# Kernel optimization log

Hardware: AMD Instinct MI355X
Metric: run time of the kernel (lower is better)

The kernel has to match this reference:

```python
import jax, jax.numpy as jnp
import numpy as np

B, N, C = 8, 2048, 512  # batch, points, channels; dk == C


def _mlp(x, W, b):
    # torch MLP helper = Linear followed by ReLU (even on the last layer)
    return jax.nn.relu(x @ W + b)


def setup_inputs() -> dict:
    key = jax.random.key(0)
    ks = jax.random.split(key, 5)
    s = 1.0 / np.sqrt(C)
    return {
        "x": jax.random.normal(ks[0], (B, N, C), dtype=jnp.float32),
        "Wh": jax.random.normal(ks[1], (C, C), dtype=jnp.float32) * s,
        "bh": jnp.zeros((C,), dtype=jnp.float32),
        "Wl": jax.random.normal(ks[2], (C, C), dtype=jnp.float32) * s,
        "bl": jnp.zeros((C,), dtype=jnp.float32),
        "Wg": jax.random.normal(ks[3], (C, C), dtype=jnp.float32) * s,
        "bg": jnp.zeros((C,), dtype=jnp.float32),
        "Wm": jax.random.normal(ks[4], (C, C), dtype=jnp.float32) * s,
        "bm": jnp.zeros((C,), dtype=jnp.float32),
    }


def reference(x, Wh, bh, Wl, bl, Wg, bg, Wm, bm):
    h = _mlp(x, Wh, bh)                      # [B, N, dk] (torch transposes; folded into einsum)
    l = _mlp(x, Wl, bl)                      # [B, N, dk]
    scores = jnp.einsum("bnd,bmd->bnm", l, h)  # [B, N, N]
    attn = jax.nn.softmax(scores, axis=-1)
    g = _mlp(x, Wg, bg)                      # [B, N, C]
    out = x + jnp.einsum("bnm,bmc->bnc", attn, g)
    return _mlp(out, Wm, bm)
```

## Files before the change

kernel.cpp:

```cpp
#include <hip/hip_runtime.h>


typedef __attribute__((ext_vector_type(4))) float f32x4;
typedef __attribute__((ext_vector_type(8))) short s16x8;
typedef __attribute__((ext_vector_type(8))) _Float16 f16x8;

typedef unsigned int u32;
typedef __attribute__((address_space(1))) const u32 gu32;
typedef __attribute__((address_space(3))) u32 lu32;

__device__ __forceinline__ void gload16(const short* g, short* l) {
  __builtin_amdgcn_global_load_lds((gu32*)g, (lu32*)l, 16, 0, 0);
}

__device__ __forceinline__ short f2h(float f) {
  _Float16 h = (_Float16)f;
  return __builtin_bit_cast(short, h);
}

#define MFMA(a, b, c) __builtin_amdgcn_mfma_f32_16x16x32_f16(a, b, c, 0, 0, 0)


__global__ __launch_bounds__(256) void conv_x_kernel(const float* __restrict__ x,
                                                     short* __restrict__ xb) {
  int i = blockIdx.x * 256 + threadIdx.x;
  const float4* xv = (const float4*)x;
  float4 a = xv[2 * i], b = xv[2 * i + 1];
  s16x8 o;
  o[0] = f2h(a.x); o[1] = f2h(a.y); o[2] = f2h(a.z); o[3] = f2h(a.w);
  o[4] = f2h(b.x); o[5] = f2h(b.y); o[6] = f2h(b.z); o[7] = f2h(b.w);
  ((s16x8*)xb)[i] = o;
}

__global__ __launch_bounds__(256) void conv_w_kernel(const float* __restrict__ Wh,
                                                     const float* __restrict__ Wl,
                                                     const float* __restrict__ Wg,
                                                     const float* __restrict__ Wm,
                                                     short* __restrict__ Wt) {
  int idx = blockIdx.x * 256 + threadIdx.x;
  int k = idx & 511, n = (idx >> 9) & 511, w = idx >> 18;
  const float* W = (w == 0) ? Wh : (w == 1) ? Wl : (w == 2) ? Wg : Wm;
  Wt[idx] = f2h(W[k * 512 + n]);
}


__global__ __launch_bounds__(256) void mlp3_kernel(const short* __restrict__ A,
                                                   const short* __restrict__ Wt_all,
                                                   const float* __restrict__ bh,
                                                   const float* __restrict__ bl,
                                                   const float* __restrict__ bg,
                                                   short* __restrict__ h,
                                                   short* __restrict__ l,
                                                   short* __restrict__ gT) {
  int z = blockIdx.z;
  const short* Wt = Wt_all + z * 262144;
  const float* bias = (z == 0) ? bh : (z == 1) ? bl : bg;

  __shared__ __align__(16) short lds_a[128 * 40];
  __shared__ __align__(16) short lds_b[128 * 40];
  int tid = threadIdx.x, lane = tid & 63, w = tid >> 6;
  int wm = w >> 1, wn = w & 1;
  int bm = blockIdx.x * 128, bn = blockIdx.y * 128;

  f32x4 acc[4][4];
#pragma unroll
  for (int mi = 0; mi < 4; ++mi)
#pragma unroll
    for (int ni = 0; ni < 4; ++ni) acc[mi][ni] = (f32x4){0.f, 0.f, 0.f, 0.f};

  for (int k0 = 0; k0 < 512; k0 += 32) {
#pragma unroll
    for (int it = 0; it < 2; ++it) {
      int chunk = tid + it * 256;
      int row = chunk >> 2, c8 = (chunk & 3) * 8;
      *(s16x8*)&lds_a[row * 40 + c8] =
          *(const s16x8*)&A[(size_t)(bm + row) * 512 + k0 + c8];
      *(s16x8*)&lds_b[row * 40 + c8] =
          *(const s16x8*)&Wt[(bn + row) * 512 + k0 + c8];
    }
    __syncthreads();
    f16x8 af[4], bfr[4];
#pragma unroll
    for (int mi = 0; mi < 4; ++mi)
      af[mi] = *(const f16x8*)&lds_a[(wm * 64 + mi * 16 + (lane & 15)) * 40 +
                                     (lane >> 4) * 8];
#pragma unroll
    for (int ni = 0; ni < 4; ++ni)
      bfr[ni] = *(const f16x8*)&lds_b[(wn * 64 + ni * 16 + (lane & 15)) * 40 +
                                      (lane >> 4) * 8];
#pragma unroll
    for (int mi = 0; mi < 4; ++mi)
#pragma unroll
      for (int ni = 0; ni < 4; ++ni) acc[mi][ni] = MFMA(af[mi], bfr[ni], acc[mi][ni]);
    __syncthreads();
  }

#pragma unroll
  for (int mi = 0; mi < 4; ++mi)
#pragma unroll
    for (int ni = 0; ni < 4; ++ni) {
      int col = bn + wn * 64 + ni * 16 + (lane & 15);
      float bv = bias[col];
#pragma unroll
      for (int r = 0; r < 4; ++r) {
        int row = bm + wm * 64 + mi * 16 + (lane >> 4) * 4 + r;
        float v = fmaxf(acc[mi][ni][r] + bv, 0.0f);
        short o = f2h(v);
        if (z == 0) h[(size_t)row * 512 + col] = o;
        else if (z == 1) l[(size_t)row * 512 + col] = o;
        else {
          int bb = row >> 11, mm = row & 2047;
          gT[((size_t)bb * 512 + col) * 2048 + mm] = o;
        }
      }
    }
}


__global__ __launch_bounds__(256, 1) void attn_kernel(const short* __restrict__ lmat,
                                                      const short* __restrict__ hmat,
                                                      const short* __restrict__ gT,
                                                      const float* __restrict__ x,
                                                      short* __restrict__ y) {
  __shared__ __align__(16) short kbuf[2][16384];
  __shared__ __align__(16) short gbuf[2][16384];
  __shared__ __align__(16) short lds_p[4][512];
  int tid = threadIdx.x, lane = tid & 63, w = tid >> 6;
  int swz = (blockIdx.x & 7) * 32 + (blockIdx.x >> 3);
  int b = swz >> 5, qt = swz & 31;
  int q0 = qt * 64 + w * 16;
  const short* lb = lmat + (size_t)b * 2048 * 512;
  const short* hb = hmat + (size_t)b * 2048 * 512;
  const short* gb = gT + (size_t)b * 512 * 2048;

  int r0 = lane & 15, g = lane >> 4;

  f16x8 qf[16];
  {
    int q = q0 + r0;
#pragma unroll
    for (int ks = 0; ks < 16; ++ks)
      qf[ks] = *(const f16x8*)&lb[(size_t)q * 512 + ks * 32 + g * 8];
  }
  f32x4 accO[32];
#pragma unroll
  for (int i = 0; i < 32; ++i) accO[i] = (f32x4){0.f, 0.f, 0.f, 0.f};
  float mrun[4], lsumL[4];
#pragma unroll
  for (int r = 0; r < 4; ++r) { mrun[r] = -3e38f; lsumL[r] = 0.f; }

  auto stage = [&](int buf, int t) {
    int key0 = t * 32;
    short* kd = &kbuf[buf][0];
    short* gd = &gbuf[buf][0];
#pragma unroll
    for (int j = 0; j < 8; ++j) {
      int wl = w * 8 + j;
      gload16(hb + (size_t)(key0 + wl) * 512 + (((lane * 16) ^ ((wl & 7) << 4)) >> 1),
              kd + wl * 512);
      int c = wl * 16 + (lane >> 2);
      gload16(gb + (size_t)c * 2048 + key0 + (lane & 3) * 8,
              gd + wl * 512);
    }
  };

  stage(0, 0);
  __syncthreads();
  int cur = 0;

  for (int kt = 0; kt < 64; ++kt) {
    if (kt < 63) stage(cur ^ 1, kt + 1);

    const short* kb = &kbuf[cur][0];
    const short* gp = &gbuf[cur][0];

    f32x4 s0 = {0.f, 0.f, 0.f, 0.f}, s1 = {0.f, 0.f, 0.f, 0.f};
#pragma unroll
    for (int ks = 0; ks < 16; ++ks) {
      f16x8 k0f = *(const f16x8*)&kb[(r0 * 512 + ks * 32 + g * 8) ^ ((r0 & 7) << 3)];
      s0 = MFMA(qf[ks], k0f, s0);
      f16x8 k1f = *(const f16x8*)&kb[((r0 + 16) * 512 + ks * 32 + g * 8) ^ ((r0 & 7) << 3)];
      s1 = MFMA(qf[ks], k1f, s1);
    }

    float mnew[4];
    bool ok = true;
#pragma unroll
    for (int r = 0; r < 4; ++r) {
      float m2 = fmaxf(s0[r], s1[r]);
#pragma unroll
      for (int m = 1; m < 16; m <<= 1) m2 = fmaxf(m2, __shfl_xor(m2, m));
      mnew[r] = fmaxf(mrun[r], m2);
      ok = ok && (m2 <= mrun[r] + 8.0f);
    }
    if (!__all((int)ok)) {
      float sc[4];
#pragma unroll
      for (int r = 0; r < 4; ++r) {
        sc[r] = __expf(mrun[r] - mnew[r]);
        mrun[r] = mnew[r];
        lsumL[r] *= sc[r];
      }
#pragma unroll
      for (int nf = 0; nf < 32; ++nf) {
        accO[nf][0] *= sc[0]; accO[nf][1] *= sc[1];
        accO[nf][2] *= sc[2]; accO[nf][3] *= sc[3];
      }
    }
#pragma unroll
    for (int r = 0; r < 4; ++r) {
      float p0 = __expf(s0[r] - mrun[r]);
      float p1 = __expf(s1[r] - mrun[r]);
      int qr = g * 4 + r;
      lds_p[w][qr * 32 + r0] = f2h(p0);
      lds_p[w][qr * 32 + 16 + r0] = f2h(p1);
      lsumL[r] += p0 + p1;
    }

    f16x8 pa = *(const f16x8*)&lds_p[w][r0 * 32 + g * 8];
#pragma unroll
    for (int nf = 0; nf < 32; ++nf) {
      f16x8 gf = *(const f16x8*)&gp[(nf * 16 + r0) * 32 + g * 8];
      accO[nf] = MFMA(pa, gf, accO[nf]);
    }

    __syncthreads();
    cur ^= 1;
  }

  float lsum[4];
#pragma unroll
  for (int r = 0; r < 4; ++r) {
    float s = lsumL[r];
#pragma unroll
    for (int m = 1; m < 16; m <<= 1) s += __shfl_xor(s, m);
    lsum[r] = s;
  }
#pragma unroll
  for (int nf = 0; nf < 32; ++nf) {
    int c = nf * 16 + r0;
#pragma unroll
    for (int r = 0; r < 4; ++r) {
      int q = q0 + g * 4 + r;
      float v = accO[nf][r] / lsum[r];
      v += x[((size_t)b * 2048 + q) * 512 + c];
      y[((size_t)b * 2048 + q) * 512 + c] = f2h(v);
    }
  }
}


__global__ __launch_bounds__(256) void final_gemm_kernel(const short* __restrict__ A,
                                                         const short* __restrict__ Wt,
                                                         const float* __restrict__ bias,
                                                         float* __restrict__ out) {
  __shared__ __align__(16) short lds_a[128 * 40];
  __shared__ __align__(16) short lds_b[128 * 40];
  int tid = threadIdx.x, lane = tid & 63, w = tid >> 6;
  int wm = w >> 1, wn = w & 1;
  int bm = blockIdx.x * 128, bn = blockIdx.y * 128;

  f32x4 acc[4][4];
#pragma unroll
  for (int mi = 0; mi < 4; ++mi)
#pragma unroll
    for (int ni = 0; ni < 4; ++ni) acc[mi][ni] = (f32x4){0.f, 0.f, 0.f, 0.f};

  for (int k0 = 0; k0 < 512; k0 += 32) {
#pragma unroll
    for (int it = 0; it < 2; ++it) {
      int chunk = tid + it * 256;
      int row = chunk >> 2, c8 = (chunk & 3) * 8;
      *(s16x8*)&lds_a[row * 40 + c8] =
          *(const s16x8*)&A[(size_t)(bm + row) * 512 + k0 + c8];
      *(s16x8*)&lds_b[row * 40 + c8] =
          *(const s16x8*)&Wt[(bn + row) * 512 + k0 + c8];
    }
    __syncthreads();
    f16x8 af[4], bfr[4];
#pragma unroll
    for (int mi = 0; mi < 4; ++mi)
      af[mi] = *(const f16x8*)&lds_a[(wm * 64 + mi * 16 + (lane & 15)) * 40 +
                                     (lane >> 4) * 8];
#pragma unroll
    for (int ni = 0; ni < 4; ++ni)
      bfr[ni] = *(const f16x8*)&lds_b[(wn * 64 + ni * 16 + (lane & 15)) * 40 +
                                      (lane >> 4) * 8];
#pragma unroll
    for (int mi = 0; mi < 4; ++mi)
#pragma unroll
      for (int ni = 0; ni < 4; ++ni) acc[mi][ni] = MFMA(af[mi], bfr[ni], acc[mi][ni]);
    __syncthreads();
  }

#pragma unroll
  for (int mi = 0; mi < 4; ++mi)
#pragma unroll
    for (int ni = 0; ni < 4; ++ni) {
      int col = bn + wn * 64 + ni * 16 + (lane & 15);
      float bv = bias[col];
#pragma unroll
      for (int r = 0; r < 4; ++r) {
        int row = bm + wm * 64 + mi * 16 + (lane >> 4) * 4 + r;
        out[(size_t)row * 512 + col] = fmaxf(acc[mi][ni][r] + bv, 0.0f);
      }
    }
}


extern "C" void kernel_launch(void* const* d_in, const int* in_sizes, int n_in,
                              void* d_out, int out_size, void* d_ws, size_t ws_size,
                              hipStream_t stream) {
  const float* x  = (const float*)d_in[0];
  const float* Wh = (const float*)d_in[1];
  const float* bh = (const float*)d_in[2];
  const float* Wl = (const float*)d_in[3];
  const float* bl = (const float*)d_in[4];
  const float* Wg = (const float*)d_in[5];
  const float* bg = (const float*)d_in[6];
  const float* Wm = (const float*)d_in[7];
  const float* bm = (const float*)d_in[8];

  char* ws = (char*)d_ws;
  const size_t SZ = 16777216;
  short* xb  = (short*)(ws + 0 * SZ);
  short* h   = (short*)(ws + 1 * SZ);
  short* l   = (short*)(ws + 2 * SZ);
  short* gT  = (short*)(ws + 3 * SZ);
  short* y   = (short*)(ws + 4 * SZ);
  short* Wt  = (short*)(ws + 5 * SZ);

  conv_x_kernel<<<4096, 256, 0, stream>>>(x, xb);
  conv_w_kernel<<<4096, 256, 0, stream>>>(Wh, Wl, Wg, Wm, Wt);
  mlp3_kernel<<<dim3(128, 4, 3), 256, 0, stream>>>(xb, Wt, bh, bl, bg, h, l, gT);
  attn_kernel<<<256, 256, 0, stream>>>(l, h, gT, x, y);
  final_gemm_kernel<<<dim3(128, 4), 256, 0, stream>>>(y, Wt + 3 * 262144, bm,
                                                      (float*)d_out);
}
```

Measured before the change: 285.9 us.

## Transpose attention MFMAs, keep P in registers, and software-pipeline QK ahead of PV

The attention kernel swaps the MFMA operand order so each lane holds one query row's scores. That reduces the row max and sum reductions to two cross-lane shuffles, and the P fragment is built in registers with packed f16 conversion plus permlane swaps instead of going through LDS. The loop is restructured to stage K two tiles ahead and to compute the next tile's QK scores while the current tile's softmax and PV run, with s_setprio hints on the MFMA sections. The epilogue now writes vectorized x loads and 4-wide stores. The trade-offs are higher register pressure from holding two score tiles and reliance on gfx950-specific permlane instructions.

```diff
diff --git a/kernel.cpp b/kernel.cpp
--- a/kernel.cpp
+++ b/kernel.cpp
@@ -3,7 +3,9 @@
 
 typedef __attribute__((ext_vector_type(4))) float f32x4;
 typedef __attribute__((ext_vector_type(8))) short s16x8;
+typedef __attribute__((ext_vector_type(4))) short s16x4;
 typedef __attribute__((ext_vector_type(8))) _Float16 f16x8;
+typedef __attribute__((ext_vector_type(4))) unsigned u32x4;
 
 typedef unsigned int u32;
 typedef __attribute__((address_space(1))) const u32 gu32;
@@ -16,6 +18,10 @@
 __device__ __forceinline__ short f2h(float f) {
   _Float16 h = (_Float16)f;
   return __builtin_bit_cast(short, h);
+}
+
+__device__ __forceinline__ unsigned pk2h(float a, float b) {
+  return __builtin_bit_cast(unsigned, __builtin_amdgcn_cvt_pkrtz(a, b));
 }
 
 #define MFMA(a, b, c) __builtin_amdgcn_mfma_f32_16x16x32_f16(a, b, c, 0, 0, 0)
@@ -124,7 +130,6 @@
                                                       short* __restrict__ y) {
   __shared__ __align__(16) short kbuf[2][16384];
   __shared__ __align__(16) short gbuf[2][16384];
-  __shared__ __align__(16) short lds_p[4][512];
   int tid = threadIdx.x, lane = tid & 63, w = tid >> 6;
   int swz = (blockIdx.x & 7) * 32 + (blockIdx.x >> 3);
   int b = swz >> 5, qt = swz & 31;
@@ -145,107 +150,114 @@
   f32x4 accO[32];
 #pragma unroll
   for (int i = 0; i < 32; ++i) accO[i] = (f32x4){0.f, 0.f, 0.f, 0.f};
-  float mrun[4], lsumL[4];
-#pragma unroll
-  for (int r = 0; r < 4; ++r) { mrun[r] = -3e38f; lsumL[r] = 0.f; }
-
-  auto stage = [&](int buf, int t) {
+  float mrun = -3e38f, lsumL = 0.f;
+
+  auto stageK = [&](int buf, int t) {
     int key0 = t * 32;
     short* kd = &kbuf[buf][0];
-    short* gd = &gbuf[buf][0];
 #pragma unroll
     for (int j = 0; j < 8; ++j) {
       int wl = w * 8 + j;
       gload16(hb + (size_t)(key0 + wl) * 512 + (((lane * 16) ^ ((wl & 7) << 4)) >> 1),
               kd + wl * 512);
+    }
+  };
+  auto stageG = [&](int buf, int t) {
+    int key0 = t * 32;
+    short* gd = &gbuf[buf][0];
+#pragma unroll
+    for (int j = 0; j < 8; ++j) {
+      int wl = w * 8 + j;
       int c = wl * 16 + (lane >> 2);
-      gload16(gb + (size_t)c * 2048 + key0 + (lane & 3) * 8,
-              gd + wl * 512);
+      gload16(gb + (size_t)c * 2048 + key0 + (lane & 3) * 8, gd + wl * 512);
     }
   };
-
-  stage(0, 0);
-  __syncthreads();
-  int cur = 0;
-
-  for (int kt = 0; kt < 64; ++kt) {
-    if (kt < 63) stage(cur ^ 1, kt + 1);
-
-    const short* kb = &kbuf[cur][0];
-    const short* gp = &gbuf[cur][0];
-
-    f32x4 s0 = {0.f, 0.f, 0.f, 0.f}, s1 = {0.f, 0.f, 0.f, 0.f};
+  auto QK = [&](int buf, f32x4& o0, f32x4& o1) {
+    const short* kb = &kbuf[buf][0];
 #pragma unroll
     for (int ks = 0; ks < 16; ++ks) {
       f16x8 k0f = *(const f16x8*)&kb[(r0 * 512 + ks * 32 + g * 8) ^ ((r0 & 7) << 3)];
-      s0 = MFMA(qf[ks], k0f, s0);
+      o0 = MFMA(k0f, qf[ks], o0);
       f16x8 k1f = *(const f16x8*)&kb[((r0 + 16) * 512 + ks * 32 + g * 8) ^ ((r0 & 7) << 3)];
-      s1 = MFMA(qf[ks], k1f, s1);
-    }
-
-    float mnew[4];
-    bool ok = true;
-#pragma unroll
-    for (int r = 0; r < 4; ++r) {
-      float m2 = fmaxf(s0[r], s1[r]);
-#pragma unroll
-      for (int m = 1; m < 16; m <<= 1) m2 = fmaxf(m2, __shfl_xor(m2, m));
-      mnew[r] = fmaxf(mrun[r], m2);
-      ok = ok && (m2 <= mrun[r] + 8.0f);
-    }
+      o1 = MFMA(k1f, qf[ks], o1);
+    }
+  };
+
+  stageK(0, 0); stageG(0, 0); stageK(1, 1);
+  __syncthreads();
+  f32x4 sc0 = {0.f, 0.f, 0.f, 0.f}, sc1 = {0.f, 0.f, 0.f, 0.f};
+  f32x4 sn0, sn1;
+  QK(0, sc0, sc1);
+  __syncthreads();
+
+  for (int t = 0; t < 64; ++t) {
+    if (t < 62) stageK(t & 1, t + 2);
+    if (t < 63) stageG((t + 1) & 1, t + 1);
+
+    sn0 = (f32x4){0.f, 0.f, 0.f, 0.f};
+    sn1 = (f32x4){0.f, 0.f, 0.f, 0.f};
+    if (t < 63) {
+      __builtin_amdgcn_s_setprio(1);
+      QK((t + 1) & 1, sn0, sn1);
+      __builtin_amdgcn_s_setprio(0);
+    }
+
+    float m2 = fmaxf(fmaxf(fmaxf(sc0[0], sc0[1]), fmaxf(sc0[2], sc0[3])),
+                     fmaxf(fmaxf(sc1[0], sc1[1]), fmaxf(sc1[2], sc1[3])));
+    m2 = fmaxf(m2, __shfl_xor(m2, 16));
+    m2 = fmaxf(m2, __shfl_xor(m2, 32));
+    bool ok = (m2 <= mrun + 8.0f);
     if (!__all((int)ok)) {
-      float sc[4];
-#pragma unroll
-      for (int r = 0; r < 4; ++r) {
-        sc[r] = __expf(mrun[r] - mnew[r]);
-        mrun[r] = mnew[r];
-        lsumL[r] *= sc[r];
-      }
-#pragma unroll
-      for (int nf = 0; nf < 32; ++nf) {
-        accO[nf][0] *= sc[0]; accO[nf][1] *= sc[1];
-        accO[nf][2] *= sc[2]; accO[nf][3] *= sc[3];
-      }
-    }
-#pragma unroll
-    for (int r = 0; r < 4; ++r) {
-      float p0 = __expf(s0[r] - mrun[r]);
-      float p1 = __expf(s1[r] - mrun[r]);
-      int qr = g * 4 + r;
-      lds_p[w][qr * 32 + r0] = f2h(p0);
-      lds_p[w][qr * 32 + 16 + r0] = f2h(p1);
-      lsumL[r] += p0 + p1;
-    }
-
-    f16x8 pa = *(const f16x8*)&lds_p[w][r0 * 32 + g * 8];
+      float mnew = fmaxf(mrun, m2);
+      float s = __expf(mrun - mnew);
+      mrun = mnew;
+      lsumL *= s;
+#pragma unroll
+      for (int nf = 0; nf < 32; ++nf) accO[nf] *= s;
+    }
+    float a0 = __expf(sc0[0] - mrun), a1 = __expf(sc0[1] - mrun);
+    float a2 = __expf(sc0[2] - mrun), a3 = __expf(sc0[3] - mrun);
+    float b0 = __expf(sc1[0] - mrun), b1 = __expf(sc1[1] - mrun);
+    float b2 = __expf(sc1[2] - mrun), b3 = __expf(sc1[3] - mrun);
+    lsumL += (a0 + a1) + (a2 + a3) + (b0 + b1) + (b2 + b3);
+
+    unsigned A0 = pk2h(a0, a1), A1 = pk2h(a2, a3);
+    unsigned B0 = pk2h(b0, b1), B1 = pk2h(b2, b3);
+    asm volatile("v_permlane32_swap_b32 %0, %1" : "+v"(A0), "+v"(B0));
+    asm volatile("v_permlane16_swap_b32 %0, %1" : "+v"(A0), "+v"(B0));
+    asm volatile("v_permlane32_swap_b32 %0, %1" : "+v"(A1), "+v"(B1));
+    asm volatile("v_permlane16_swap_b32 %0, %1" : "+v"(A1), "+v"(B1));
+    u32x4 pw = {A0, A1, B0, B1};
+    f16x8 pfrag = __builtin_bit_cast(f16x8, pw);
+
+    const short* gp = &gbuf[t & 1][0];
+    __builtin_amdgcn_s_setprio(1);
 #pragma unroll
     for (int nf = 0; nf < 32; ++nf) {
       f16x8 gf = *(const f16x8*)&gp[(nf * 16 + r0) * 32 + g * 8];
-      accO[nf] = MFMA(pa, gf, accO[nf]);
-    }
-
-    __syncthreads();
-    cur ^= 1;
-  }
-
-  float lsum[4];
-#pragma unroll
-  for (int r = 0; r < 4; ++r) {
-    float s = lsumL[r];
-#pragma unroll
-    for (int m = 1; m < 16; m <<= 1) s += __shfl_xor(s, m);
-    lsum[r] = s;
-  }
+      accO[nf] = MFMA(gf, pfrag, accO[nf]);
+    }
+    __builtin_amdgcn_s_setprio(0);
+
+    __syncthreads();
+    sc0 = sn0; sc1 = sn1;
+  }
+
+  float ls = lsumL;
+  ls += __shfl_xor(ls, 16);
+  ls += __shfl_xor(ls, 32);
+  float inv = 1.0f / ls;
+  int q = q0 + r0;
 #pragma unroll
   for (int nf = 0; nf < 32; ++nf) {
-    int c = nf * 16 + r0;
-#pragma unroll
-    for (int r = 0; r < 4; ++r) {
-      int q = q0 + g * 4 + r;
-      float v = accO[nf][r] / lsum[r];
-      v += x[((size_t)b * 2048 + q) * 512 + c];
-      y[((size_t)b * 2048 + q) * 512 + c] = f2h(v);
-    }
+    int d0 = nf * 16 + g * 4;
+    float4 xr = *(const float4*)&x[((size_t)b * 2048 + q) * 512 + d0];
+    s16x4 o;
+    o[0] = f2h(accO[nf][0] * inv + xr.x);
+    o[1] = f2h(accO[nf][1] * inv + xr.y);
+    o[2] = f2h(accO[nf][2] * inv + xr.z);
+    o[3] = f2h(accO[nf][3] * inv + xr.w);
+    *(s16x4*)&y[((size_t)b * 2048 + q) * 512 + d0] = o;
   }
 }
 
```

After: 286.9 us. Within noise of the previous version (+0.4%).
